# Optimization experiments

Measured on AMD Instinct MI355X. Metric: run time of the kernel, lower is better.

The kernel has to match this reference:

```python
import jax, jax.numpy as jnp
import numpy as np

B, S, D = 8, 1024, 2048          # batch, seq_len, model dim (q_features == kv_features)
H, HD = 16, 128                   # num_heads, head_dim; H*HD == hidden == 2048


def setup_inputs() -> dict:
    key = jax.random.key(0)
    ks = jax.random.split(key, 6)
    fan_in = 1.0 / np.sqrt(D)     # variance_scaling(1.0, 'fan_in') style init scale
    return {
        "inputs_q": jax.random.normal(ks[0], (B, S, D), jnp.float32),
        "inputs_kv": jax.random.normal(ks[1], (B, S, D), jnp.float32),
        "Wq": jax.random.normal(ks[2], (D, H * HD), jnp.float32) * fan_in,
        "Wk": jax.random.normal(ks[3], (D, H * HD), jnp.float32) * fan_in,
        "Wv": jax.random.normal(ks[4], (D, H * HD), jnp.float32) * fan_in,
        "Wo": jax.random.normal(ks[5], (H * HD, D), jnp.float32) * (1.0 / np.sqrt(H * HD)),
    }


def reference(inputs_q, inputs_kv, Wq, Wk, Wv, Wo):
    b, sq, _ = inputs_q.shape
    skv = inputs_kv.shape[1]
    # QKV projections (DenseGeneral, no bias), reshape to heads
    # scale_attn_logits=True -> query scaled by 1/sqrt(head_dim)
    q = (inputs_q @ Wq).reshape(b, sq, H, HD) * (1.0 / np.sqrt(HD))
    k = (inputs_kv @ Wk).reshape(b, skv, H, HD)
    v = (inputs_kv @ Wv).reshape(b, skv, H, HD)
    # dot-product attention core: [b, h, q, k] scores -> softmax -> context
    scores = jnp.einsum('bqhd,bkhd->bhqk', q, k)
    attn = jax.nn.softmax(scores, axis=-1)
    ctx = jnp.einsum('bhqk,bkhd->bqhd', attn, v).reshape(b, sq, H * HD)
    # output projection back to q_features
    return ctx @ Wo
```

## Files before the change

### kernel.cpp

```cpp
#include <hip/hip_runtime.h>
#include <cstdint>
#include <cstddef>

#define B_  8
#define S_  1024
#define D_  2048
#define H_  16
#define HD_ 128

typedef __bf16 bf16x8 __attribute__((ext_vector_type(8)));
typedef float  f32x4  __attribute__((ext_vector_type(4)));

__device__ __forceinline__ unsigned short f2b(float f) {
    unsigned int u = __float_as_uint(f);
    unsigned int r = (u + 0x7fffu + ((u >> 16) & 1u)) >> 16;
    return (unsigned short)r;
}

__device__ __forceinline__ void gl2lds16(const void* g, void* l) {
    __builtin_amdgcn_global_load_lds(
        (const __attribute__((address_space(1))) void*)g,
        (__attribute__((address_space(3))) void*)l, 16, 0, 0);
}

__global__ void cvt_f32_bf16(const float* __restrict__ src,
                             unsigned short* __restrict__ dst, int n4) {
    int i = blockIdx.x * blockDim.x + threadIdx.x;
    if (i >= n4) return;
    float4 v = ((const float4*)src)[i];
    ushort4 o;
    o.x = f2b(v.x); o.y = f2b(v.y); o.z = f2b(v.z); o.w = f2b(v.w);
    ((ushort4*)dst)[i] = o;
}

__global__ void wtrans(const float* __restrict__ W, unsigned short* __restrict__ Wt) {
    __shared__ float tile[32][33];
    int bx = blockIdx.x, by = blockIdx.y;
    int tx = threadIdx.x, ty = threadIdx.y;
#pragma unroll
    for (int i = 0; i < 4; i++)
        tile[ty + i * 8][tx] = W[(size_t)(by * 32 + ty + i * 8) * D_ + bx * 32 + tx];
    __syncthreads();
#pragma unroll
    for (int i = 0; i < 4; i++)
        Wt[(size_t)(bx * 32 + ty + i * 8) * D_ + by * 32 + tx] = f2b(tile[tx][ty + i * 8]);
}

__global__ void vtrans(const unsigned short* __restrict__ V, unsigned short* __restrict__ Vt) {
    __shared__ unsigned short tile[32][33];
    int bh = blockIdx.z;
    int b = bh >> 4, h = bh & 15;
    int tx = threadIdx.x, ty = threadIdx.y;
    int s0 = blockIdx.x * 32, hd0 = blockIdx.y * 32;
#pragma unroll
    for (int i = 0; i < 4; i++)
        tile[ty + i * 8][tx] = V[(size_t)(b * S_ + s0 + ty + i * 8) * D_ + h * HD_ + hd0 + tx];
    __syncthreads();
#pragma unroll
    for (int i = 0; i < 4; i++)
        Vt[((size_t)bh * HD_ + hd0 + ty + i * 8) * S_ + s0 + tx] = tile[tx][ty + i * 8];
}

template <bool OUTF>
__global__ void __launch_bounds__(256, 2)
gemm_bt2(const unsigned short* __restrict__ A0, const unsigned short* __restrict__ A1,
         const unsigned short* __restrict__ A2,
         const unsigned short* __restrict__ B0, const unsigned short* __restrict__ B1,
         const unsigned short* __restrict__ B2,
         unsigned short* __restrict__ o0, unsigned short* __restrict__ o1,
         unsigned short* __restrict__ o2, float* __restrict__ oF,
         float s0, float s1, float s2) {
    __shared__ unsigned short sA[256 * 64];
    __shared__ unsigned short sB[128 * 64];
    const int tid = threadIdx.x;
    const int w = tid >> 6, lane = tid & 63;
    const int l15 = lane & 15, lhi = lane >> 4;
    const int region = blockIdx.x >> 4;
    const unsigned short* A  = region == 0 ? A0 : (region == 1 ? A1 : A2);
    const unsigned short* Bt = region == 0 ? B0 : (region == 1 ? B1 : B2);
    unsigned short* outB     = region == 0 ? o0 : (region == 1 ? o1 : o2);
    const float scale        = region == 0 ? s0 : (region == 1 ? s1 : s2);
    const int mBase = blockIdx.y * 256;
    const int nBase = (blockIdx.x & 15) * 128;
    const int wm = (w >> 1) * 128, wn = (w & 1) * 64;

    int xoff[2];
#pragma unroll
    for (int ks = 0; ks < 2; ks++)
        xoff[ks] = (((ks * 4 + lhi) ^ (l15 & 7)) * 8);

    f32x4 acc[8][4] = {};

    for (int kb = 0; kb < D_; kb += 64) {
        __syncthreads();
#pragma unroll
        for (int p = 0; p < 8; p++) {
            int c = p * 256 + tid;
            int row = c >> 3, pc = c & 7;
            int j = pc ^ (row & 7);
            gl2lds16(A + (size_t)(mBase + row) * D_ + kb + j * 8, sA + c * 8);
        }
#pragma unroll
        for (int p = 0; p < 4; p++) {
            int c = p * 256 + tid;
            int row = c >> 3, pc = c & 7;
            int j = pc ^ (row & 7);
            gl2lds16(Bt + (size_t)(nBase + row) * D_ + kb + j * 8, sB + c * 8);
        }
        __syncthreads();

#pragma unroll
        for (int ks = 0; ks < 2; ks++) {
            bf16x8 bF[4];
#pragma unroll
            for (int j = 0; j < 4; j++)
                bF[j] = *(const bf16x8*)(sB + (wn + j * 16 + l15) * 64 + xoff[ks]);
#pragma unroll
            for (int i = 0; i < 8; i++) {
                bf16x8 aF = *(const bf16x8*)(sA + (wm + i * 16 + l15) * 64 + xoff[ks]);
#pragma unroll
                for (int j = 0; j < 4; j++)
                    acc[i][j] = __builtin_amdgcn_mfma_f32_16x16x32_bf16(aF, bF[j], acc[i][j], 0, 0, 0);
            }
        }
    }

#pragma unroll
    for (int i = 0; i < 8; i++) {
#pragma unroll
        for (int j = 0; j < 4; j++) {
#pragma unroll
            for (int r = 0; r < 4; r++) {
                int row = mBase + wm + i * 16 + lhi * 4 + r;
                int col = nBase + wn + j * 16 + l15;
                float v = acc[i][j][r] * scale;
                if (OUTF) oF[(size_t)row * D_ + col] = v;
                else      outB[(size_t)row * D_ + col] = f2b(v);
            }
        }
    }
}

#define PSTR 72
__global__ void __launch_bounds__(256, 2)
attn(const unsigned short* __restrict__ Q,
     const unsigned short* __restrict__ Kb,
     const unsigned short* __restrict__ Vt,
     unsigned short* __restrict__ ctx) {
    __shared__ unsigned short sK[64 * 128];
    __shared__ unsigned short sV[128 * 64];
    __shared__ unsigned short sP[4 * 32 * PSTR];
    const int tid = threadIdx.x;
    const int w = tid >> 6, lane = tid & 63;
    const int l15 = lane & 15, lhi = lane >> 4;
    const int qt = blockIdx.x, h = blockIdx.y, b = blockIdx.z;
    const unsigned short* Qp = Q  + (size_t)b * S_ * D_ + h * HD_;
    const unsigned short* Kp = Kb + (size_t)b * S_ * D_ + h * HD_;
    const unsigned short* Vp = Vt + (size_t)(b * H_ + h) * HD_ * S_;
    const int q0 = qt * 128 + w * 32;

    int xoff[2];
#pragma unroll
    for (int ks = 0; ks < 2; ks++)
        xoff[ks] = (((ks * 4 + lhi) ^ (l15 & 7)) * 8);

    bf16x8 qF[2][4];
#pragma unroll
    for (int i = 0; i < 2; i++)
#pragma unroll
        for (int kk = 0; kk < 4; kk++)
            qF[i][kk] = *(const bf16x8*)(Qp + (size_t)(q0 + i * 16 + l15) * D_ + kk * 32 + lhi * 8);

    f32x4 o4[2][8] = {};
    float lrun[2][4] = {};
    unsigned short* sPw = sP + w * 32 * PSTR;

    for (int kt = 0; kt < S_ / 64; kt++) {
        __syncthreads();
#pragma unroll
        for (int p = 0; p < 4; p++) {
            int c = p * 256 + tid;
            {
                int row = c >> 4, pc = c & 15;
                int j = pc ^ (row & 7);
                gl2lds16(Kp + (size_t)(kt * 64 + row) * D_ + j * 8, sK + c * 8);
            }
            {
                int row = c >> 3, pc = c & 7;
                int j = pc ^ (row & 7);
                gl2lds16(Vp + (size_t)row * S_ + kt * 64 + j * 8, sV + c * 8);
            }
        }
        __syncthreads();

        f32x4 s4[2][4] = {};
#pragma unroll
        for (int j = 0; j < 4; j++) {
#pragma unroll
            for (int kk = 0; kk < 4; kk++) {
                bf16x8 bF = *(const bf16x8*)(sK + (j * 16 + l15) * 128 + ((kk * 4 + lhi) ^ (l15 & 7)) * 8);
#pragma unroll
                for (int i = 0; i < 2; i++)
                    s4[i][j] = __builtin_amdgcn_mfma_f32_16x16x32_bf16(qF[i][kk], bF, s4[i][j], 0, 0, 0);
            }
        }

#pragma unroll
        for (int i = 0; i < 2; i++) {
#pragma unroll
            for (int r = 0; r < 4; r++) {
                int prow = i * 16 + lhi * 4 + r;
                float ps = 0.f;
#pragma unroll
                for (int j = 0; j < 4; j++) {
                    float pv = exp2f(s4[i][j][r]);
                    ps += pv;
                    sPw[prow * PSTR + j * 16 + l15] = f2b(pv);
                }
                lrun[i][r] += ps;
            }
        }

#pragma unroll
        for (int k2 = 0; k2 < 2; k2++) {
            bf16x8 pF[2];
#pragma unroll
            for (int i = 0; i < 2; i++)
                pF[i] = *(const bf16x8*)(sPw + (i * 16 + l15) * PSTR + k2 * 32 + lhi * 8);
#pragma unroll
            for (int nt = 0; nt < 8; nt++) {
                bf16x8 vF = *(const bf16x8*)(sV + (nt * 16 + l15) * 64 + xoff[k2]);
#pragma unroll
                for (int i = 0; i < 2; i++)
                    o4[i][nt] = __builtin_amdgcn_mfma_f32_16x16x32_bf16(pF[i], vF, o4[i][nt], 0, 0, 0);
            }
        }
    }

#pragma unroll
    for (int i = 0; i < 2; i++)
#pragma unroll
        for (int r = 0; r < 4; r++) {
            float s = lrun[i][r];
#pragma unroll
            for (int msk = 1; msk < 16; msk <<= 1) s += __shfl_xor(s, msk);
            lrun[i][r] = 1.0f / s;
        }
#pragma unroll
    for (int i = 0; i < 2; i++)
#pragma unroll
        for (int nt = 0; nt < 8; nt++)
#pragma unroll
            for (int r = 0; r < 4; r++) {
                size_t row = (size_t)b * S_ + q0 + i * 16 + lhi * 4 + r;
                ctx[row * D_ + h * HD_ + nt * 16 + l15] = f2b(o4[i][nt][r] * lrun[i][r]);
            }
}

extern "C" void kernel_launch(void* const* d_in, const int* in_sizes, int n_in,
                              void* d_out, int out_size, void* d_ws, size_t ws_size,
                              hipStream_t stream) {
    const float* Xq  = (const float*)d_in[0];
    const float* Xkv = (const float*)d_in[1];
    const float* Wq  = (const float*)d_in[2];
    const float* Wk  = (const float*)d_in[3];
    const float* Wv  = (const float*)d_in[4];
    const float* Wo  = (const float*)d_in[5];
    float* out = (float*)d_out;

    char* ws = (char*)d_ws;
    const size_t XSZ = (size_t)B_ * S_ * D_ * 2;
    const size_t WSZ = (size_t)D_ * D_ * 2;
    unsigned short* XqB  = (unsigned short*)(ws);
    unsigned short* XkvB = (unsigned short*)(ws + XSZ);
    unsigned short* WqT  = (unsigned short*)(ws + 2 * XSZ);
    unsigned short* WkT  = (unsigned short*)(ws + 2 * XSZ + WSZ);
    unsigned short* WvT  = (unsigned short*)(ws + 2 * XSZ + 2 * WSZ);
    unsigned short* WoT  = (unsigned short*)(ws + 2 * XSZ + 3 * WSZ);
    unsigned short* Qb   = (unsigned short*)(ws + 3 * XSZ);
    unsigned short* Kb   = (unsigned short*)(ws + 4 * XSZ);
    unsigned short* Vb   = (unsigned short*)(ws + 5 * XSZ);
    unsigned short* VtB  = XkvB;
    unsigned short* ctxB = XqB;

    const int n4 = B_ * S_ * D_ / 4;
    cvt_f32_bf16<<<n4 / 256, 256, 0, stream>>>(Xq,  XqB,  n4);
    cvt_f32_bf16<<<n4 / 256, 256, 0, stream>>>(Xkv, XkvB, n4);

    dim3 tb(32, 8);
    wtrans<<<dim3(64, 64), tb, 0, stream>>>(Wq, WqT);
    wtrans<<<dim3(64, 64), tb, 0, stream>>>(Wk, WkT);
    wtrans<<<dim3(64, 64), tb, 0, stream>>>(Wv, WvT);
    wtrans<<<dim3(64, 64), tb, 0, stream>>>(Wo, WoT);

    const float qscale = 1.44269504088896f / 11.313708498984761f;

    gemm_bt2<false><<<dim3(48, 32), 256, 0, stream>>>(
        XqB, XkvB, XkvB, WqT, WkT, WvT, Qb, Kb, Vb, nullptr, qscale, 1.0f, 1.0f);

    vtrans<<<dim3(S_ / 32, HD_ / 32, B_ * H_), tb, 0, stream>>>(Vb, VtB);

    attn<<<dim3(S_ / 128, H_, B_), 256, 0, stream>>>(Qb, Kb, VtB, ctxB);

    gemm_bt2<true><<<dim3(16, 32), 256, 0, stream>>>(
        ctxB, ctxB, ctxB, WoT, WoT, WoT, nullptr, nullptr, nullptr, out, 1.0f, 1.0f, 1.0f);
}
```

Baseline: 603.2 us.

## Rewrite projection GEMMs as 256x256-tile, 512-thread, ping-pong pipelined kernel

```diff
diff --git a/kernel.cpp b/kernel.cpp
--- a/kernel.cpp
+++ b/kernel.cpp
@@ -7,6 +7,7 @@
 #define D_  2048
 #define H_  16
 #define HD_ 128
+#define NT_ (D_ / 64)
 
 typedef __bf16 bf16x8 __attribute__((ext_vector_type(8)));
 typedef float  f32x4  __attribute__((ext_vector_type(4)));
@@ -61,79 +62,125 @@
         Vt[((size_t)bh * HD_ + hd0 + ty + i * 8) * S_ + s0 + tx] = tile[tx][ty + i * 8];
 }
 
+#define STAGE1(TN, KH, SRC, DST) do {                                              \
+    const int _kb = (TN) * 64 + (KH) * 32;                                         \
+    _Pragma("unroll")                                                              \
+    for (int _p = 0; _p < 2; _p++) {                                               \
+        int _c = _p * 512 + tid;                                                   \
+        int _row = _c >> 2;                                                        \
+        int _j = (_c & 3) ^ ((_row >> 1) & 3);                                     \
+        gl2lds16(SRC + (size_t)_row * D_ + _kb + _j * 8, DST + _c * 8);            \
+    }                                                                              \
+} while (0)
+
+#define PHASE(SAP, SBP, MH, READB, TN, KH2, SSRC, SDST, VM) do {                   \
+    asm volatile("" ::: "memory");                                                 \
+    if (READB) {                                                                   \
+        _Pragma("unroll")                                                          \
+        for (int j = 0; j < 4; j++)                                                \
+            bF[j] = *(const bf16x8*)(SAP##_unused, &SBP[(wn + j * 16 + l15) * 32 + swz]); \
+    }                                                                              \
+    bf16x8 aF[4];                                                                  \
+    _Pragma("unroll")                                                              \
+    for (int i = 0; i < 4; i++)                                                    \
+        aF[i] = *(const bf16x8*)(&SAP[(wm + (MH) * 64 + i * 16 + l15) * 32 + swz]);\
+    STAGE1(TN, KH2, SSRC, SDST);                                                   \
+    asm volatile("" ::: "memory");                                                 \
+    __builtin_amdgcn_s_barrier();                                                  \
+    asm volatile("s_waitcnt lgkmcnt(0)" ::: "memory");                             \
+    __builtin_amdgcn_sched_barrier(0);                                             \
+    __builtin_amdgcn_s_setprio(1);                                                 \
+    _Pragma("unroll")                                                              \
+    for (int i = 0; i < 4; i++)                                                    \
+        _Pragma("unroll")                                                          \
+        for (int j = 0; j < 4; j++)                                                \
+            acc[(MH) * 4 + i][j] =                                                 \
+                __builtin_amdgcn_mfma_f32_16x16x32_bf16(aF[i], bF[j],              \
+                                                        acc[(MH) * 4 + i][j], 0, 0, 0); \
+    __builtin_amdgcn_s_setprio(0);                                                 \
+    if (VM) asm volatile("s_waitcnt vmcnt(4)" ::: "memory");                       \
+    asm volatile("" ::: "memory");                                                 \
+    __builtin_amdgcn_s_barrier();                                                  \
+} while (0)
+
+#define sA00_unused 0
+#define sA01_unused 0
+#define sA10_unused 0
+#define sA11_unused 0
+
 template <bool OUTF>
-__global__ void __launch_bounds__(256, 2)
-gemm_bt2(const unsigned short* __restrict__ A0, const unsigned short* __restrict__ A1,
+__global__ void __launch_bounds__(512, 2)
+gemm_bt3(const unsigned short* __restrict__ A0, const unsigned short* __restrict__ A1,
          const unsigned short* __restrict__ A2,
          const unsigned short* __restrict__ B0, const unsigned short* __restrict__ B1,
          const unsigned short* __restrict__ B2,
          unsigned short* __restrict__ o0, unsigned short* __restrict__ o1,
          unsigned short* __restrict__ o2, float* __restrict__ oF,
          float s0, float s1, float s2) {
-    __shared__ unsigned short sA[256 * 64];
-    __shared__ unsigned short sB[128 * 64];
+    __shared__ __align__(16) unsigned short sA00[256 * 32], sA01[256 * 32];
+    __shared__ __align__(16) unsigned short sA10[256 * 32], sA11[256 * 32];
+    __shared__ __align__(16) unsigned short sB00[256 * 32], sB01[256 * 32];
+    __shared__ __align__(16) unsigned short sB10[256 * 32], sB11[256 * 32];
+
     const int tid = threadIdx.x;
     const int w = tid >> 6, lane = tid & 63;
     const int l15 = lane & 15, lhi = lane >> 4;
-    const int region = blockIdx.x >> 4;
+
+    const int nwgx = gridDim.x;
+    const int nwg = nwgx * gridDim.y;
+    const int lin = blockIdx.y * nwgx + blockIdx.x;
+    const int per = nwg >> 3;
+    const int sw = (lin & 7) * per + (lin >> 3);
+    const int bx = sw % nwgx, by = sw / nwgx;
+
+    const int region = bx >> 3;
     const unsigned short* A  = region == 0 ? A0 : (region == 1 ? A1 : A2);
     const unsigned short* Bt = region == 0 ? B0 : (region == 1 ? B1 : B2);
     unsigned short* outB     = region == 0 ? o0 : (region == 1 ? o1 : o2);
     const float scale        = region == 0 ? s0 : (region == 1 ? s1 : s2);
-    const int mBase = blockIdx.y * 256;
-    const int nBase = (blockIdx.x & 15) * 128;
-    const int wm = (w >> 1) * 128, wn = (w & 1) * 64;
-
-    int xoff[2];
-#pragma unroll
-    for (int ks = 0; ks < 2; ks++)
-        xoff[ks] = (((ks * 4 + lhi) ^ (l15 & 7)) * 8);
+    const int mBase = by * 256;
+    const int nBase = (bx & 7) * 256;
+    const int wm = (w >> 2) * 128, wn = (w & 3) * 64;
+
+    const unsigned short* Ap = A  + (size_t)mBase * D_;
+    const unsigned short* Bp = Bt + (size_t)nBase * D_;
+
+    const int swz = (lhi ^ ((l15 >> 1) & 3)) * 8;
 
     f32x4 acc[8][4] = {};
-
-    for (int kb = 0; kb < D_; kb += 64) {
-        __syncthreads();
-#pragma unroll
-        for (int p = 0; p < 8; p++) {
-            int c = p * 256 + tid;
-            int row = c >> 3, pc = c & 7;
-            int j = pc ^ (row & 7);
-            gl2lds16(A + (size_t)(mBase + row) * D_ + kb + j * 8, sA + c * 8);
-        }
-#pragma unroll
-        for (int p = 0; p < 4; p++) {
-            int c = p * 256 + tid;
-            int row = c >> 3, pc = c & 7;
-            int j = pc ^ (row & 7);
-            gl2lds16(Bt + (size_t)(nBase + row) * D_ + kb + j * 8, sB + c * 8);
-        }
-        __syncthreads();
-
-#pragma unroll
-        for (int ks = 0; ks < 2; ks++) {
-            bf16x8 bF[4];
-#pragma unroll
-            for (int j = 0; j < 4; j++)
-                bF[j] = *(const bf16x8*)(sB + (wn + j * 16 + l15) * 64 + xoff[ks]);
-#pragma unroll
-            for (int i = 0; i < 8; i++) {
-                bf16x8 aF = *(const bf16x8*)(sA + (wm + i * 16 + l15) * 64 + xoff[ks]);
-#pragma unroll
-                for (int j = 0; j < 4; j++)
-                    acc[i][j] = __builtin_amdgcn_mfma_f32_16x16x32_bf16(aF, bF[j], acc[i][j], 0, 0, 0);
-            }
-        }
+    bf16x8 bF[4];
+
+    STAGE1(0, 0, Ap, sA00);
+    STAGE1(0, 0, Bp, sB00);
+    STAGE1(0, 1, Ap, sA01);
+    STAGE1(0, 1, Bp, sB01);
+    asm volatile("s_waitcnt vmcnt(4)" ::: "memory");
+    asm volatile("" ::: "memory");
+    __builtin_amdgcn_s_barrier();
+
+#pragma unroll 1
+    for (int tt = 0; tt < NT_; tt += 2) {
+        const int t1 = tt + 1;
+        const int t2 = (tt + 2) & (NT_ - 1);
+        PHASE(sA00, sB00, 0, true , t1, 0, Ap, sA10, false);
+        PHASE(sA00, sB00, 1, false, t1, 0, Bp, sB10, true );
+        PHASE(sA01, sB01, 0, true , t1, 1, Ap, sA11, false);
+        PHASE(sA01, sB01, 1, false, t1, 1, Bp, sB11, true );
+        PHASE(sA10, sB10, 0, true , t2, 0, Ap, sA00, false);
+        PHASE(sA10, sB10, 1, false, t2, 0, Bp, sB00, true );
+        PHASE(sA11, sB11, 0, true , t2, 1, Ap, sA01, false);
+        PHASE(sA11, sB11, 1, false, t2, 1, Bp, sB01, true );
     }
 
 #pragma unroll
-    for (int i = 0; i < 8; i++) {
+    for (int ai = 0; ai < 8; ai++) {
 #pragma unroll
         for (int j = 0; j < 4; j++) {
 #pragma unroll
             for (int r = 0; r < 4; r++) {
-                int row = mBase + wm + i * 16 + lhi * 4 + r;
+                int row = mBase + wm + ai * 16 + lhi * 4 + r;
                 int col = nBase + wn + j * 16 + l15;
-                float v = acc[i][j][r] * scale;
+                float v = acc[ai][j][r] * scale;
                 if (OUTF) oF[(size_t)row * D_ + col] = v;
                 else      outB[(size_t)row * D_ + col] = f2b(v);
             }
@@ -198,10 +245,10 @@
         for (int j = 0; j < 4; j++) {
 #pragma unroll
             for (int kk = 0; kk < 4; kk++) {
-                bf16x8 bF = *(const bf16x8*)(sK + (j * 16 + l15) * 128 + ((kk * 4 + lhi) ^ (l15 & 7)) * 8);
+                bf16x8 bFk = *(const bf16x8*)(sK + (j * 16 + l15) * 128 + ((kk * 4 + lhi) ^ (l15 & 7)) * 8);
 #pragma unroll
                 for (int i = 0; i < 2; i++)
-                    s4[i][j] = __builtin_amdgcn_mfma_f32_16x16x32_bf16(qF[i][kk], bF, s4[i][j], 0, 0, 0);
+                    s4[i][j] = __builtin_amdgcn_mfma_f32_16x16x32_bf16(qF[i][kk], bFk, s4[i][j], 0, 0, 0);
             }
         }
 
@@ -295,13 +342,13 @@
 
     const float qscale = 1.44269504088896f / 11.313708498984761f;
 
-    gemm_bt2<false><<<dim3(48, 32), 256, 0, stream>>>(
+    gemm_bt3<false><<<dim3(24, 32), 512, 0, stream>>>(
         XqB, XkvB, XkvB, WqT, WkT, WvT, Qb, Kb, Vb, nullptr, qscale, 1.0f, 1.0f);
 
     vtrans<<<dim3(S_ / 32, HD_ / 32, B_ * H_), tb, 0, stream>>>(Vb, VtB);
 
     attn<<<dim3(S_ / 128, H_, B_), 256, 0, stream>>>(Qb, Kb, VtB, ctxB);
 
-    gemm_bt2<true><<<dim3(16, 32), 256, 0, stream>>>(
+    gemm_bt3<true><<<dim3(8, 32), 512, 0, stream>>>(
         ctxB, ctxB, ctxB, WoT, WoT, WoT, nullptr, nullptr, nullptr, out, 1.0f, 1.0f, 1.0f);
 }
```

After: 638.0 us. +5.8%, slower.

## Double-buffer K tiles and overlap loads with MFMA in attention kernel

Applied to the files above, without the earlier changes.

```diff
diff --git a/kernel.cpp b/kernel.cpp
--- a/kernel.cpp
+++ b/kernel.cpp
@@ -142,12 +142,97 @@
 }
 
 #define PSTR 72
+
+#define ATT_STAGE_V(KT) do {                                                       \
+    _Pragma("unroll")                                                              \
+    for (int _p = 0; _p < 4; _p++) {                                               \
+        int _c = _p * 256 + tid;                                                   \
+        int _row = _c >> 3, _pc = _c & 7;                                          \
+        int _j = _pc ^ (_row & 7);                                                 \
+        gl2lds16(Vp + (size_t)_row * S_ + (KT) * 64 + _j * 8, sV + _c * 8);        \
+    }                                                                              \
+} while (0)
+
+#define ATT_STAGE_K(KT, BUF) do {                                                  \
+    _Pragma("unroll")                                                              \
+    for (int _p = 0; _p < 4; _p++) {                                               \
+        int _c = _p * 256 + tid;                                                   \
+        int _row = _c >> 4, _pc = _c & 15;                                         \
+        int _j = _pc ^ (_row & 7);                                                 \
+        gl2lds16(Kp + (size_t)((KT) * 64 + _row) * D_ + _j * 8, (BUF) + _c * 8);   \
+    }                                                                              \
+} while (0)
+
+#define ATT_BODY(KT, SKC, SKN) do {                                                \
+    ATT_STAGE_V(KT);                                                               \
+    ATT_STAGE_K(((KT) + 1) & 15, SKN);                                             \
+    asm volatile("s_waitcnt vmcnt(8)");                                            \
+    __builtin_amdgcn_sched_barrier(0);                                             \
+    __builtin_amdgcn_s_barrier();                                                  \
+    __builtin_amdgcn_sched_barrier(0);                                             \
+    f32x4 s4[2][4] = {};                                                           \
+    __builtin_amdgcn_s_setprio(1);                                                 \
+    _Pragma("unroll")                                                              \
+    for (int j = 0; j < 4; j++) {                                                  \
+        _Pragma("unroll")                                                          \
+        for (int kk = 0; kk < 4; kk++) {                                           \
+            bf16x8 bFk = *(const bf16x8*)(SKC + (j * 16 + l15) * 128 +             \
+                                          ((kk * 4 + lhi) ^ (l15 & 7)) * 8);       \
+            _Pragma("unroll")                                                      \
+            for (int i = 0; i < 2; i++)                                            \
+                s4[i][j] = __builtin_amdgcn_mfma_f32_16x16x32_bf16(qF[i][kk], bFk, \
+                                                                   s4[i][j], 0, 0, 0); \
+        }                                                                          \
+    }                                                                              \
+    __builtin_amdgcn_s_setprio(0);                                                 \
+    _Pragma("unroll")                                                              \
+    for (int i = 0; i < 2; i++) {                                                  \
+        _Pragma("unroll")                                                          \
+        for (int r = 0; r < 4; r++) {                                              \
+            int prow = i * 16 + lhi * 4 + r;                                       \
+            float ps = 0.f;                                                        \
+            _Pragma("unroll")                                                      \
+            for (int j = 0; j < 4; j++) {                                          \
+                float pv = exp2f(s4[i][j][r]);                                     \
+                ps += pv;                                                          \
+                sPw[prow * PSTR + j * 16 + l15] = f2b(pv);                         \
+            }                                                                      \
+            lrun[i][r] += ps;                                                      \
+        }                                                                          \
+    }                                                                              \
+    asm volatile("s_waitcnt vmcnt(4)");                                            \
+    __builtin_amdgcn_sched_barrier(0);                                             \
+    __builtin_amdgcn_s_barrier();                                                  \
+    __builtin_amdgcn_sched_barrier(0);                                             \
+    __builtin_amdgcn_s_setprio(1);                                                 \
+    _Pragma("unroll")                                                              \
+    for (int k2 = 0; k2 < 2; k2++) {                                               \
+        bf16x8 pF[2];                                                              \
+        _Pragma("unroll")                                                          \
+        for (int i = 0; i < 2; i++)                                                \
+            pF[i] = *(const bf16x8*)(sPw + (i * 16 + l15) * PSTR + k2 * 32 + lhi * 8); \
+        _Pragma("unroll")                                                          \
+        for (int nt = 0; nt < 8; nt++) {                                           \
+            bf16x8 vF = *(const bf16x8*)(sV + (nt * 16 + l15) * 64 + xoff[k2]);    \
+            _Pragma("unroll")                                                      \
+            for (int i = 0; i < 2; i++)                                            \
+                o4[i][nt] = __builtin_amdgcn_mfma_f32_16x16x32_bf16(pF[i], vF,     \
+                                                                    o4[i][nt], 0, 0, 0); \
+        }                                                                          \
+    }                                                                              \
+    __builtin_amdgcn_s_setprio(0);                                                 \
+    __builtin_amdgcn_sched_barrier(0);                                             \
+    __builtin_amdgcn_s_barrier();                                                  \
+    __builtin_amdgcn_sched_barrier(0);                                             \
+} while (0)
+
 __global__ void __launch_bounds__(256, 2)
 attn(const unsigned short* __restrict__ Q,
      const unsigned short* __restrict__ Kb,
      const unsigned short* __restrict__ Vt,
      unsigned short* __restrict__ ctx) {
-    __shared__ unsigned short sK[64 * 128];
+    __shared__ unsigned short sK0[64 * 128];
+    __shared__ unsigned short sK1[64 * 128];
     __shared__ unsigned short sV[128 * 64];
     __shared__ unsigned short sP[4 * 32 * PSTR];
     const int tid = threadIdx.x;
@@ -171,71 +256,24 @@
         for (int kk = 0; kk < 4; kk++)
             qF[i][kk] = *(const bf16x8*)(Qp + (size_t)(q0 + i * 16 + l15) * D_ + kk * 32 + lhi * 8);
 
+    __builtin_amdgcn_sched_barrier(0);
+    asm volatile("s_waitcnt vmcnt(0)");
+    __builtin_amdgcn_sched_barrier(0);
+
     f32x4 o4[2][8] = {};
     float lrun[2][4] = {};
     unsigned short* sPw = sP + w * 32 * PSTR;
 
-    for (int kt = 0; kt < S_ / 64; kt++) {
-        __syncthreads();
-#pragma unroll
-        for (int p = 0; p < 4; p++) {
-            int c = p * 256 + tid;
-            {
-                int row = c >> 4, pc = c & 15;
-                int j = pc ^ (row & 7);
-                gl2lds16(Kp + (size_t)(kt * 64 + row) * D_ + j * 8, sK + c * 8);
-            }
-            {
-                int row = c >> 3, pc = c & 7;
-                int j = pc ^ (row & 7);
-                gl2lds16(Vp + (size_t)row * S_ + kt * 64 + j * 8, sV + c * 8);
-            }
-        }
-        __syncthreads();
-
-        f32x4 s4[2][4] = {};
-#pragma unroll
-        for (int j = 0; j < 4; j++) {
-#pragma unroll
-            for (int kk = 0; kk < 4; kk++) {
-                bf16x8 bF = *(const bf16x8*)(sK + (j * 16 + l15) * 128 + ((kk * 4 + lhi) ^ (l15 & 7)) * 8);
-#pragma unroll
-                for (int i = 0; i < 2; i++)
-                    s4[i][j] = __builtin_amdgcn_mfma_f32_16x16x32_bf16(qF[i][kk], bF, s4[i][j], 0, 0, 0);
-            }
-        }
-
-#pragma unroll
-        for (int i = 0; i < 2; i++) {
-#pragma unroll
-            for (int r = 0; r < 4; r++) {
-                int prow = i * 16 + lhi * 4 + r;
-                float ps = 0.f;
-#pragma unroll
-                for (int j = 0; j < 4; j++) {
-                    float pv = exp2f(s4[i][j][r]);
-                    ps += pv;
-                    sPw[prow * PSTR + j * 16 + l15] = f2b(pv);
-                }
-                lrun[i][r] += ps;
-            }
-        }
-
-#pragma unroll
-        for (int k2 = 0; k2 < 2; k2++) {
-            bf16x8 pF[2];
-#pragma unroll
-            for (int i = 0; i < 2; i++)
-                pF[i] = *(const bf16x8*)(sPw + (i * 16 + l15) * PSTR + k2 * 32 + lhi * 8);
-#pragma unroll
-            for (int nt = 0; nt < 8; nt++) {
-                bf16x8 vF = *(const bf16x8*)(sV + (nt * 16 + l15) * 64 + xoff[k2]);
-#pragma unroll
-                for (int i = 0; i < 2; i++)
-                    o4[i][nt] = __builtin_amdgcn_mfma_f32_16x16x32_bf16(pF[i], vF, o4[i][nt], 0, 0, 0);
-            }
-        }
+    ATT_STAGE_K(0, sK0);
+
+#pragma unroll 1
+    for (int kt = 0; kt < S_ / 64; kt += 2) {
+        ATT_BODY(kt,     sK0, sK1);
+        ATT_BODY(kt + 1, sK1, sK0);
     }
+
+    asm volatile("s_waitcnt vmcnt(0)");
+    __builtin_amdgcn_sched_barrier(0);
 
 #pragma unroll
     for (int i = 0; i < 2; i++)
```

New measurement: 606.5 us. About the same (+0.6%).
